# Kernel tuning notes

Measured on AMD Instinct MI355X. Metric: run time of the kernel, lower is better.

Reference implementation:

```python
import jax, jax.numpy as jnp
import numpy as np

B, D_IN, EMB = 8192, 4000, 96
H0, H1 = 2048, 1024
NB, NC, OPT = 8, 8, 32
NE = NB * NC  # 64 experts (total contests)


def setup_inputs() -> dict:
    key = jax.random.key(0)
    ks = jax.random.split(key, 10)
    scale = lambda fan_in: jnp.sqrt(2.0 / fan_in)  # kaiming_normal-ish
    return {
        "inputs": jax.random.normal(ks[0], (B, D_IN), dtype=jnp.float32),
        "emb_table": jax.random.normal(ks[1], (NE, EMB), dtype=jnp.float32) * scale(EMB),
        "W0": jax.random.normal(ks[2], (D_IN + EMB, H0), dtype=jnp.float32) * scale(D_IN + EMB),
        "b0": jnp.zeros((H0,), dtype=jnp.float32),
        "W1": jax.random.normal(ks[3], (H0, H1), dtype=jnp.float32) * scale(H0),
        "b1": jnp.zeros((H1,), dtype=jnp.float32),
        "We": jax.random.normal(ks[4], (NE, H1, OPT), dtype=jnp.float32) * scale(H1),
        "be": jnp.zeros((NE, OPT), dtype=jnp.float32),
        "ballot_number": jax.random.randint(ks[5], (B,), 0, NB, dtype=jnp.int32),
        "contest_number": jax.random.randint(ks[6], (B,), 0, NC, dtype=jnp.int32),
        "batches": B,
    }


def reference(inputs, emb_table, W0, b0, W1, b1, We, be,
              ballot_number, contest_number, batches):
    # flat expert index per sample: index_of[ballot][contest] with equal-size ballots
    expert = ballot_number * NC + contest_number                  # [B]
    x = inputs.reshape(batches, -1)                               # [B, D_IN]
    emb = emb_table[expert]                                       # [B, EMB] (gather)
    h = jnp.concatenate([emb, x], axis=1)                         # [B, D_IN+EMB]
    h = jax.nn.relu(h @ W0 + b0)                                  # fc0 (dropout = id at eval)
    h = jax.nn.relu(h @ W1 + b1)                                  # fc1
    # per-sample routed linear: gather expert weights, batched matvec
    out = jnp.einsum("bd,bdo->bo", h, We[expert]) + be[expert]    # [B, OPT]
    return jax.nn.sigmoid(out)
```

## Files before the change

### kernel.cpp

```cpp
#include <hip/hip_runtime.h>
#include <math.h>

typedef __attribute__((ext_vector_type(8))) short short8;
typedef __attribute__((ext_vector_type(4))) float f32x4;

#define B_SZ 8192
#define D_INN 4000
#define EMBD 96
#define H0D 2048
#define H1D 1024
#define KDIM 4096

__device__ __forceinline__ unsigned short f2bf(float f) {
  union { float f; unsigned u; } v; v.f = f;
  unsigned r = v.u + 0x7FFFu + ((v.u >> 16) & 1u);
  return (unsigned short)(r >> 16);
}
__device__ __forceinline__ float bf2f(unsigned short h) {
  union { unsigned u; float f; } v; v.u = ((unsigned)h) << 16;
  return v.f;
}
__device__ __forceinline__ void gld_lds16(const void* g, void* l) {
  __builtin_amdgcn_global_load_lds(
      (const __attribute__((address_space(1))) unsigned int*)g,
      (__attribute__((address_space(3))) unsigned int*)l, 16, 0, 0);
}

__global__ __launch_bounds__(256) void transpose_cvt(
    const float* __restrict__ in, unsigned short* __restrict__ out, int R, int C) {
  __shared__ float tile[32][33];
  int c0 = blockIdx.x * 32, r0 = blockIdx.y * 32;
  int tc = threadIdx.x & 31, tr = threadIdx.x >> 5;
#pragma unroll
  for (int i = 0; i < 4; ++i) {
    int r = tr + i * 8;
    tile[r][tc] = in[(size_t)(r0 + r) * C + (c0 + tc)];
  }
  __syncthreads();
#pragma unroll
  for (int i = 0; i < 4; ++i) {
    int rr = tr + i * 8;
    out[(size_t)(c0 + rr) * R + (r0 + tc)] = f2bf(tile[tc][rr]);
  }
}

__global__ __launch_bounds__(256) void build_A(
    const float* __restrict__ inputs, const float* __restrict__ emb,
    const int* __restrict__ ballot, const int* __restrict__ contest,
    unsigned short* __restrict__ A) {
  int gid = blockIdx.x * 256 + threadIdx.x;
  int b = gid >> 9, c = gid & 511;
  const float* src;
  if (c < EMBD / 8) {
    int e = ballot[b] * 8 + contest[b];
    src = emb + (size_t)e * EMBD + c * 8;
  } else {
    src = inputs + (size_t)b * D_INN + (c - EMBD / 8) * 8;
  }
  float4 v0 = *(const float4*)src;
  float4 v1 = *(const float4*)(src + 4);
  unsigned short r[8];
  r[0] = f2bf(v0.x); r[1] = f2bf(v0.y); r[2] = f2bf(v0.z); r[3] = f2bf(v0.w);
  r[4] = f2bf(v1.x); r[5] = f2bf(v1.y); r[6] = f2bf(v1.z); r[7] = f2bf(v1.w);
  *reinterpret_cast<short8*>(A + (size_t)b * KDIM + c * 8) =
      *reinterpret_cast<const short8*>(r);
}

template <int MREP>
__global__ __launch_bounds__(512, 2) void gemm_nt_pipe(
    const unsigned short* __restrict__ A, const unsigned short* __restrict__ Bt,
    const float* __restrict__ bias, unsigned short* __restrict__ C,
    int K, int N, int NBN) {
  constexpr int BM  = MREP * 32;
  constexpr int AI  = MREP / 4;
  constexpr int ASH = BM * 32;
  constexpr int MH  = MREP / 2;
  __shared__ unsigned short lds[3 * ASH + 3 * 8192];

  const int tid = threadIdx.x;
  const int w = tid >> 6, l = tid & 63;
  const int lr = l & 15, kg = l >> 4;
  const int wm = w >> 2, wn = w & 3;

  int swz = (blockIdx.x & 7) * ((int)gridDim.x >> 3) + ((int)blockIdx.x >> 3);
  const int bm = swz / NBN, bn = swz - bm * NBN;
  const int NT = K >> 5;

  const int rg = l >> 2;
  const int sl = ((l & 3) ^ ((l >> 3) & 3)) * 8;
  const unsigned short* ga[AI];
#pragma unroll
  for (int i = 0; i < AI; ++i)
    ga[i] = A + (size_t)(bm * BM + (i * 8 + w) * 16 + rg) * K + sl;
  const unsigned short* gb0 = Bt + (size_t)(bn * 256 + w * 16 + rg) * K + sl;
  const unsigned short* gb1 = gb0 + (size_t)128 * K;

  const int xo = (kg ^ ((lr >> 1) & 3)) << 4;
  const int aoff = (wm * (MREP * 16) + lr) * 64 + xo;
  const int boff = (wn * 64 + lr) * 64 + xo;

  f32x4 acc[MREP][4] = {};

  auto stageA = [&](int t, int rbuf) {
    unsigned short* la = lds + rbuf * ASH + w * 512;
    const int ko = t * 32;
#pragma unroll
    for (int i = 0; i < AI; ++i) gld_lds16(ga[i] + ko, la + i * 4096);
  };
  auto stageB = [&](int t, int rbuf) {
    unsigned short* lb = lds + 3 * ASH + rbuf * 8192 + w * 512;
    const int ko = t * 32;
    gld_lds16(gb0 + ko, lb);
    gld_lds16(gb1 + ko, lb + 4096);
  };

#define WAIT_VM_STEADY() do { \
    if constexpr (AI == 2) asm volatile("s_waitcnt vmcnt(4)" ::: "memory"); \
    else                   asm volatile("s_waitcnt vmcnt(3)" ::: "memory"); \
  } while (0)

  stageA(0, 0); stageB(0, 0);
  stageA(1, 1); stageB(1, 1);
  WAIT_VM_STEADY();
  __builtin_amdgcn_s_barrier();

  int rb = 0;
  for (int t = 0; t < NT; ++t) {
    int rb2 = rb + 2; if (rb2 >= 3) rb2 -= 3;
    const char* pa = (const char*)lds + rb * (ASH * 2) + aoff;
    const char* pb = (const char*)lds + 3 * (ASH * 2) + rb * 16384 + boff;

    short8 a0[MH], bfr[4];
#pragma unroll
    for (int mi = 0; mi < MH; ++mi) a0[mi] = *(const short8*)(pa + mi * 1024);
#pragma unroll
    for (int ni = 0; ni < 4; ++ni)  bfr[ni] = *(const short8*)(pb + ni * 1024);
    if (t + 2 < NT) stageA(t + 2, rb2);
    asm volatile("s_waitcnt lgkmcnt(0)" ::: "memory");
    __builtin_amdgcn_s_barrier();
    __builtin_amdgcn_s_setprio(1);
#pragma unroll
    for (int mi = 0; mi < MH; ++mi)
#pragma unroll
      for (int ni = 0; ni < 4; ++ni)
        acc[mi][ni] = __builtin_amdgcn_mfma_f32_16x16x32_bf16(
            a0[mi], bfr[ni], acc[mi][ni], 0, 0, 0);
    __builtin_amdgcn_s_setprio(0);

    short8 a1[MH];
#pragma unroll
    for (int mi = 0; mi < MH; ++mi) a1[mi] = *(const short8*)(pa + (MH + mi) * 1024);
    if (t + 2 < NT) {
      stageB(t + 2, rb2);
      asm volatile("s_waitcnt lgkmcnt(0)" ::: "memory");
      WAIT_VM_STEADY();
      __builtin_amdgcn_s_barrier();
    } else if (t + 1 < NT) {
      asm volatile("s_waitcnt lgkmcnt(0)" ::: "memory");
      asm volatile("s_waitcnt vmcnt(0)" ::: "memory");
      __builtin_amdgcn_s_barrier();
    } else {
      asm volatile("s_waitcnt lgkmcnt(0)" ::: "memory");
    }
    __builtin_amdgcn_s_setprio(1);
#pragma unroll
    for (int mi = 0; mi < MH; ++mi)
#pragma unroll
      for (int ni = 0; ni < 4; ++ni)
        acc[MH + mi][ni] = __builtin_amdgcn_mfma_f32_16x16x32_bf16(
            a1[mi], bfr[ni], acc[MH + mi][ni], 0, 0, 0);
    __builtin_amdgcn_s_setprio(0);

    rb = rb + 1; if (rb >= 3) rb = 0;
  }

#pragma unroll
  for (int mi = 0; mi < MREP; ++mi) {
    const int row0 = bm * BM + wm * (MREP * 16) + mi * 16 + kg * 4;
#pragma unroll
    for (int ni = 0; ni < 4; ++ni) {
      const int col = bn * 256 + wn * 64 + ni * 16 + lr;
      const float bv = bias[col];
#pragma unroll
      for (int j = 0; j < 4; ++j) {
        float v = acc[mi][ni][j] + bv;
        v = v > 0.f ? v : 0.f;
        C[(size_t)(row0 + j) * N + col] = f2bf(v);
      }
    }
  }
#undef WAIT_VM_STEADY
}

__global__ __launch_bounds__(256) void expert_head(
    const unsigned short* __restrict__ h1, const float* __restrict__ We,
    const float* __restrict__ be, const int* __restrict__ ballot,
    const int* __restrict__ contest, float* __restrict__ out) {
  int b = blockIdx.x * 4 + (threadIdx.x >> 6);
  int lane = threadIdx.x & 63;
  int o = lane & 31, half = lane >> 5;
  int e = ballot[b] * 8 + contest[b];
  const unsigned short* hrow = h1 + (size_t)b * H1D + half * 512;
  const float* wb = We + ((size_t)e * H1D + half * 512) * 32 + o;
  float acc = 0.f;
  for (int d0 = 0; d0 < 512; d0 += 8) {
    short8 hv = *reinterpret_cast<const short8*>(&hrow[d0]);
#pragma unroll
    for (int j = 0; j < 8; ++j)
      acc = fmaf(bf2f((unsigned short)hv[j]), wb[(size_t)(d0 + j) * 32], acc);
  }
  acc += __shfl_xor(acc, 32, 64);
  if (half == 0) {
    float x = acc + be[e * 32 + o];
    out[(size_t)b * 32 + o] = 1.f / (1.f + expf(-x));
  }
}

extern "C" void kernel_launch(void* const* d_in, const int* in_sizes, int n_in,
                              void* d_out, int out_size, void* d_ws, size_t ws_size,
                              hipStream_t stream) {
  const float* inputs = (const float*)d_in[0];
  const float* emb    = (const float*)d_in[1];
  const float* W0     = (const float*)d_in[2];
  const float* b0     = (const float*)d_in[3];
  const float* W1     = (const float*)d_in[4];
  const float* b1     = (const float*)d_in[5];
  const float* We     = (const float*)d_in[6];
  const float* be     = (const float*)d_in[7];
  const int* ballot   = (const int*)d_in[8];
  const int* contest  = (const int*)d_in[9];
  float* out = (float*)d_out;

  char* ws = (char*)d_ws;
  unsigned short* A   = (unsigned short*)(ws);
  unsigned short* W0t = (unsigned short*)(ws + 67108864);
  unsigned short* h0  = (unsigned short*)(ws + 83886080);
  unsigned short* W1t = (unsigned short*)(ws + 117440512);
  unsigned short* h1  = (unsigned short*)(ws + 121634816);

  dim3 blk(256);
  transpose_cvt<<<dim3(H0D / 32, KDIM / 32, 1), blk, 0, stream>>>(W0, W0t, KDIM, H0D);
  transpose_cvt<<<dim3(H1D / 32, H0D / 32, 1), blk, 0, stream>>>(W1, W1t, H0D, H1D);
  build_A<<<dim3(B_SZ * 512 / 256), blk, 0, stream>>>(inputs, emb, ballot, contest, A);
  gemm_nt_pipe<8><<<dim3((B_SZ / 256) * (H0D / 256)), dim3(512), 0, stream>>>(
      A, W0t, b0, h0, KDIM, H0D, H0D / 256);
  gemm_nt_pipe<4><<<dim3((B_SZ / 128) * (H1D / 256)), dim3(512), 0, stream>>>(
      h0, W1t, b1, h1, H0D, H1D, H1D / 256);
  expert_head<<<dim3(B_SZ / 4), blk, 0, stream>>>(h1, We, be, ballot, contest, out);
}
```

Baseline: 264.3 us.

## Group samples by expert and compute routed head with bf16 MFMA

Replaces the per-sample scalar FMA expert head with a kernel that launches one block per expert. Each block gathers the indices of the samples routed to that expert and runs bf16 MFMA tiles against a transposed bf16 copy of the expert weights. A new transpose kernel converts We to bf16 in the free A workspace after the first GEMM. This removes the repeated fp32 weight reads per sample, but it caps each expert at 1024 samples, uses only 64 blocks, and every block scans all 8192 routing entries.

```diff
diff --git a/kernel.cpp b/kernel.cpp
--- a/kernel.cpp
+++ b/kernel.cpp
@@ -11,6 +11,8 @@
 #define H1D 1024
 #define KDIM 4096
 
+#define MFMA_BF16 __builtin_amdgcn_mfma_f32_16x16x32_bf16
+
 __device__ __forceinline__ unsigned short f2bf(float f) {
   union { float f; unsigned u; } v; v.f = f;
   unsigned r = v.u + 0x7FFFu + ((v.u >> 16) & 1u);
@@ -41,6 +43,26 @@
   for (int i = 0; i < 4; ++i) {
     int rr = tr + i * 8;
     out[(size_t)(c0 + rr) * R + (r0 + tc)] = f2bf(tile[tc][rr]);
+  }
+}
+
+__global__ __launch_bounds__(256) void transpose_cvt_we(
+    const float* __restrict__ in, unsigned short* __restrict__ out) {
+  __shared__ float tile[32][33];
+  const int e = blockIdx.y, r0 = blockIdx.x * 32;
+  const float* src = in + (size_t)e * 32768;
+  unsigned short* dst = out + (size_t)e * 32768;
+  int tc = threadIdx.x & 31, tr = threadIdx.x >> 5;
+#pragma unroll
+  for (int i = 0; i < 4; ++i) {
+    int r = tr + i * 8;
+    tile[r][tc] = src[(size_t)(r0 + r) * 32 + tc];
+  }
+  __syncthreads();
+#pragma unroll
+  for (int i = 0; i < 4; ++i) {
+    int rr = tr + i * 8;
+    dst[(size_t)rr * H1D + r0 + tc] = f2bf(tile[tc][rr]);
   }
 }
 
@@ -143,8 +165,7 @@
     for (int mi = 0; mi < MH; ++mi)
 #pragma unroll
       for (int ni = 0; ni < 4; ++ni)
-        acc[mi][ni] = __builtin_amdgcn_mfma_f32_16x16x32_bf16(
-            a0[mi], bfr[ni], acc[mi][ni], 0, 0, 0);
+        acc[mi][ni] = MFMA_BF16(a0[mi], bfr[ni], acc[mi][ni], 0, 0, 0);
     __builtin_amdgcn_s_setprio(0);
 
     short8 a1[MH];
@@ -167,8 +188,7 @@
     for (int mi = 0; mi < MH; ++mi)
 #pragma unroll
       for (int ni = 0; ni < 4; ++ni)
-        acc[MH + mi][ni] = __builtin_amdgcn_mfma_f32_16x16x32_bf16(
-            a1[mi], bfr[ni], acc[MH + mi][ni], 0, 0, 0);
+        acc[MH + mi][ni] = MFMA_BF16(a1[mi], bfr[ni], acc[MH + mi][ni], 0, 0, 0);
     __builtin_amdgcn_s_setprio(0);
 
     rb = rb + 1; if (rb >= 3) rb = 0;
@@ -192,27 +212,58 @@
 #undef WAIT_VM_STEADY
 }
 
-__global__ __launch_bounds__(256) void expert_head(
-    const unsigned short* __restrict__ h1, const float* __restrict__ We,
+__global__ __launch_bounds__(256) void expert_head_mfma(
+    const unsigned short* __restrict__ h1, const unsigned short* __restrict__ Wet,
     const float* __restrict__ be, const int* __restrict__ ballot,
     const int* __restrict__ contest, float* __restrict__ out) {
-  int b = blockIdx.x * 4 + (threadIdx.x >> 6);
-  int lane = threadIdx.x & 63;
-  int o = lane & 31, half = lane >> 5;
-  int e = ballot[b] * 8 + contest[b];
-  const unsigned short* hrow = h1 + (size_t)b * H1D + half * 512;
-  const float* wb = We + ((size_t)e * H1D + half * 512) * 32 + o;
-  float acc = 0.f;
-  for (int d0 = 0; d0 < 512; d0 += 8) {
-    short8 hv = *reinterpret_cast<const short8*>(&hrow[d0]);
-#pragma unroll
-    for (int j = 0; j < 8; ++j)
-      acc = fmaf(bf2f((unsigned short)hv[j]), wb[(size_t)(d0 + j) * 32], acc);
-  }
-  acc += __shfl_xor(acc, 32, 64);
-  if (half == 0) {
-    float x = acc + be[e * 32 + o];
-    out[(size_t)b * 32 + o] = 1.f / (1.f + expf(-x));
+  const int e = blockIdx.x;
+  __shared__ unsigned short sidx[1024];
+  __shared__ int scnt;
+  if (threadIdx.x == 0) scnt = 0;
+  __syncthreads();
+  for (int i = threadIdx.x; i < B_SZ; i += 256)
+    if (ballot[i] * 8 + contest[i] == e) {
+      int p = atomicAdd(&scnt, 1);
+      if (p < 1024) sidx[p] = (unsigned short)i;
+    }
+  __syncthreads();
+  const int cnt = min(scnt, 1024);
+  const int w = threadIdx.x >> 6, l = threadIdx.x & 63;
+  const int lr = l & 15, kg = l >> 4;
+  const unsigned short* wbase = Wet + (size_t)e * 32768;
+  for (int c0 = w * 32; c0 < cnt; c0 += 128) {
+    const int ns = min(32, cnt - c0);
+    f32x4 acc[2][2] = {};
+    int ridx[2];
+#pragma unroll
+    for (int mi = 0; mi < 2; ++mi) {
+      int rr = mi * 16 + lr;
+      ridx[mi] = sidx[c0 + (rr < ns ? rr : 0)];
+    }
+#pragma unroll 4
+    for (int kk = 0; kk < 32; ++kk) {
+      short8 a0 = *(const short8*)(h1 + (size_t)ridx[0] * H1D + kk * 32 + kg * 8);
+      short8 a1 = *(const short8*)(h1 + (size_t)ridx[1] * H1D + kk * 32 + kg * 8);
+      short8 b0 = *(const short8*)(wbase + (size_t)lr * H1D + kk * 32 + kg * 8);
+      short8 b1 = *(const short8*)(wbase + (size_t)(16 + lr) * H1D + kk * 32 + kg * 8);
+      acc[0][0] = MFMA_BF16(a0, b0, acc[0][0], 0, 0, 0);
+      acc[0][1] = MFMA_BF16(a0, b1, acc[0][1], 0, 0, 0);
+      acc[1][0] = MFMA_BF16(a1, b0, acc[1][0], 0, 0, 0);
+      acc[1][1] = MFMA_BF16(a1, b1, acc[1][1], 0, 0, 0);
+    }
+#pragma unroll
+    for (int mi = 0; mi < 2; ++mi)
+#pragma unroll
+      for (int ni = 0; ni < 2; ++ni)
+#pragma unroll
+        for (int j = 0; j < 4; ++j) {
+          int row = mi * 16 + kg * 4 + j;
+          int col = ni * 16 + lr;
+          if (row < ns) {
+            float x = acc[mi][ni][j] + be[e * 32 + col];
+            out[(size_t)sidx[c0 + row] * 32 + col] = 1.f / (1.f + expf(-x));
+          }
+        }
   }
 }
 
@@ -237,6 +288,7 @@
   unsigned short* h0  = (unsigned short*)(ws + 83886080);
   unsigned short* W1t = (unsigned short*)(ws + 117440512);
   unsigned short* h1  = (unsigned short*)(ws + 121634816);
+  unsigned short* Wet = (unsigned short*)(ws);
 
   dim3 blk(256);
   transpose_cvt<<<dim3(H0D / 32, KDIM / 32, 1), blk, 0, stream>>>(W0, W0t, KDIM, H0D);
@@ -244,7 +296,8 @@
   build_A<<<dim3(B_SZ * 512 / 256), blk, 0, stream>>>(inputs, emb, ballot, contest, A);
   gemm_nt_pipe<8><<<dim3((B_SZ / 256) * (H0D / 256)), dim3(512), 0, stream>>>(
       A, W0t, b0, h0, KDIM, H0D, H0D / 256);
+  transpose_cvt_we<<<dim3(32, 64), blk, 0, stream>>>(We, Wet);
   gemm_nt_pipe<4><<<dim3((B_SZ / 128) * (H1D / 256)), dim3(512), 0, stream>>>(
       h0, W1t, b1, h1, H0D, H1D, H1D / 256);
-  expert_head<<<dim3(B_SZ / 4), blk, 0, stream>>>(h1, We, be, ballot, contest, out);
-}
+  expert_head_mfma<<<dim3(64), blk, 0, stream>>>(h1, Wet, be, ballot, contest, out);
+}
```

Result: faster. 243.2 us (-8.0%).
